# Kernel tuning notes

Measured on AMD Instinct MI355X. Metric: run time of the kernel, lower is better.

The kernel has to match this reference:

```python
import jax, jax.numpy as jnp
import numpy as np

B, S_IMG, S_TXT, S_BOK = 1, 2048, 512, 4
DM, H, DH, R = 3072, 24, 128, 16
LORA_SCALE, LORA_ALPHA, BOKEH_SCALE = 1.0, 16.0, 1.0
EPS = 1e-6


def _rms_norm(x, w):
    # normalize over head_dim (last axis), Flux RMSNorm eps=1e-6
    var = jnp.mean(jnp.square(x), axis=-1, keepdims=True)
    return x * jax.lax.rsqrt(var + EPS) * w


def _lora(x, w_down, w_up):
    # LoRALinear: up(down(x)) * alpha/rank
    return (x @ w_down.T) @ w_up.T * (LORA_ALPHA / R)


def _apply_rope(x, cos, sin):
    # x: [B,H,S,D]; cos/sin: [S,D]; diffusers use_real=True, unbind_dim=-1 (interleaved pairs)
    x1 = x[..., 0::2]
    x2 = x[..., 1::2]
    rot = jnp.stack([-x2, x1], axis=-1).reshape(x.shape)
    return x * cos[None, None] + rot * sin[None, None]


def _sdpa(q, k, v):
    # q:[B,H,Sq,D] k,v:[B,H,Sk,D]
    scale = 1.0 / jnp.sqrt(jnp.asarray(q.shape[-1], q.dtype))
    scores = jnp.einsum('bhqd,bhkd->bhqk', q, k) * scale
    p = jax.nn.softmax(scores, axis=-1)
    return jnp.einsum('bhqk,bhkd->bhqd', p, v)


def setup_inputs() -> dict:
    key = jax.random.key(0)
    ks = jax.random.split(key, 40)
    std = 0.02
    d = {}
    d['hidden_states'] = jax.random.normal(ks[0], (B, S_IMG, DM), jnp.float32)
    d['encoder_hidden_states'] = jax.random.normal(ks[1], (B, S_TXT, DM), jnp.float32)
    d['bokeh_embeds'] = jax.random.normal(ks[2], (B, S_BOK, DM), jnp.float32)
    theta = jax.random.uniform(ks[3], (S_TXT + S_IMG, DH // 2), jnp.float32) * 2 * np.pi
    theta = jnp.repeat(theta, 2, axis=-1)  # interleaved pairs share angle
    d['rope_cos'] = jnp.cos(theta)
    d['rope_sin'] = jnp.sin(theta)
    # base attention params
    for i, nm in enumerate(['Wq', 'Wk', 'Wv', 'Waq', 'Wak', 'Wav', 'Wo', 'Wao']):
        d[nm] = jax.random.normal(ks[4 + i], (DM, DM), jnp.float32) * std
    for i, nm in enumerate(['bq', 'bk', 'bv', 'baq', 'bak', 'bav', 'bo', 'bao']):
        d[nm] = jax.random.normal(ks[12 + i], (DM,), jnp.float32) * std
    for i, nm in enumerate(['norm_q_w', 'norm_k_w', 'norm_aq_w', 'norm_ak_w']):
        d[nm] = 1.0 + jax.random.normal(ks[20 + i], (DH,), jnp.float32) * std
    # LoRA adapters (up weights random, not zero, for nontrivial math)
    for i, nm in enumerate(['kb_down', 'vb_down', 'qadp_down', 'kadp_down']):
        d[nm] = jax.random.normal(ks[24 + i], (R, DM), jnp.float32) * (1.0 / R)
    for i, nm in enumerate(['kb_up', 'vb_up', 'qadp_up', 'kadp_up']):
        d[nm] = jax.random.normal(ks[28 + i], (DM, R), jnp.float32) * std
    return d


def reference(hidden_states, encoder_hidden_states, bokeh_embeds, rope_cos, rope_sin,
              Wq, Wk, Wv, Waq, Wak, Wav, Wo, Wao,
              bq, bk, bv, baq, bak, bav, bo, bao,
              norm_q_w, norm_k_w, norm_aq_w, norm_ak_w,
              kb_down, vb_down, qadp_down, kadp_down,
              kb_up, vb_up, qadp_up, kadp_up):
    Bsz = encoder_hidden_states.shape[0]

    def heads(x):  # [B,S,DM] -> [B,H,S,DH]
        return x.reshape(Bsz, -1, H, DH).transpose(0, 2, 1, 3)

    q = hidden_states @ Wq.T + bq
    k = hidden_states @ Wk.T + bk
    v = hidden_states @ Wv.T + bv
    q = q + LORA_SCALE * _lora(q, qadp_down, qadp_up)
    k = k + LORA_SCALE * _lora(k, kadp_down, kadp_up)
    q, k, v = heads(q), heads(k), heads(v)
    q = _rms_norm(q, norm_q_w)
    k = _rms_norm(k, norm_k_w)

    eq = heads(encoder_hidden_states @ Waq.T + baq)
    ek = heads(encoder_hidden_states @ Wak.T + bak)
    ev = heads(encoder_hidden_states @ Wav.T + bav)
    eq = _rms_norm(eq, norm_aq_w)
    ek = _rms_norm(ek, norm_ak_w)

    q = jnp.concatenate([eq, q], axis=2)
    k = jnp.concatenate([ek, k], axis=2)
    v = jnp.concatenate([ev, v], axis=2)

    q = _apply_rope(q, rope_cos, rope_sin)
    k = _apply_rope(k, rope_cos, rope_sin)

    out = _sdpa(q, k, v)  # [B,H,S,DH]
    out = out.transpose(0, 2, 1, 3).reshape(Bsz, -1, H * DH)

    # bokeh pass
    kd = heads(_lora(bokeh_embeds, kb_down, kb_up))
    vd = heads(_lora(bokeh_embeds, vb_down, vb_up))
    cam = _sdpa(q, kd, vd).transpose(0, 2, 1, 3).reshape(Bsz, -1, H * DH)
    out = out + BOKEH_SCALE * cam

    enc_out = out[:, :S_TXT]
    img_out = out[:, S_TXT:]
    img_out = img_out @ Wo.T + bo
    enc_out = enc_out @ Wao.T + bao
    return (img_out, enc_out)
```

## Files before the change

### kernel.cpp

```cpp
#include <hip/hip_runtime.h>

#define DMDL 3072
#define SEQ  2560
#define STXT 512
#define HEADS 24
#define DHD  128
#define WB9 9437184

typedef float f32x4 __attribute__((ext_vector_type(4)));
typedef __bf16 bf16x8 __attribute__((ext_vector_type(8)));
typedef unsigned short u16x4 __attribute__((ext_vector_type(4)));

static __device__ __forceinline__ unsigned short f2bf(float f) {
  unsigned u = __float_as_uint(f);
  u += 0x7fffu + ((u >> 16) & 1u);
  return (unsigned short)(u >> 16);
}

static __device__ __forceinline__ float fexp2(float x) {
  return __builtin_amdgcn_exp2f(x);
}

static __device__ __forceinline__ void gload16(const unsigned short* g, unsigned short* l) {
  __builtin_amdgcn_global_load_lds(
      (const __attribute__((address_space(1))) unsigned int*)g,
      (__attribute__((address_space(3))) unsigned int*)l, 16, 0, 0);
}

__global__ __launch_bounds__(256) void convf2b_kernel(
    const float* __restrict__ src, unsigned short* __restrict__ dst) {
  const int idx4 = blockIdx.x * 256 + threadIdx.x;
  float4 v = *(const float4*)(src + (size_t)idx4 * 4);
  u16x4 b = { f2bf(v.x), f2bf(v.y), f2bf(v.z), f2bf(v.w) };
  *(u16x4*)(dst + (size_t)idx4 * 4) = b;
}

__global__ __launch_bounds__(256) void convw_kernel(
    const float* __restrict__ s0, const float* __restrict__ s1,
    const float* __restrict__ s2, unsigned short* __restrict__ dst) {
  const float* src = (blockIdx.y == 0) ? s0 : (blockIdx.y == 1) ? s1 : s2;
  const size_t idx4 = (size_t)blockIdx.x * 256 + threadIdx.x;
  float4 v = *(const float4*)(src + idx4 * 4);
  u16x4 b = { f2bf(v.x), f2bf(v.y), f2bf(v.z), f2bf(v.w) };
  *(u16x4*)(dst + (size_t)blockIdx.y * WB9 + idx4 * 4) = b;
}

__device__ __forceinline__ void gemm_body(
    const unsigned short* __restrict__ A, const unsigned short* __restrict__ Bw,
    const float* __restrict__ bias, float* __restrict__ C,
    int row0, int col0) {
  __shared__ unsigned short Al[128][64];
  __shared__ unsigned short Bl[128][64];
  const int t = threadIdx.x, w = t >> 6, l = t & 63;
  const int wr = (w >> 1) << 6, wc = (w & 1) << 6;
  const int l15 = l & 15, lg = l >> 4;
  f32x4 acc[4][4];
#pragma unroll
  for (int i = 0; i < 4; i++)
#pragma unroll
    for (int j = 0; j < 4; j++) acc[i][j] = (f32x4){0.f, 0.f, 0.f, 0.f};

  for (int k0 = 0; k0 < DMDL; k0 += 64) {
    __syncthreads();
#pragma unroll
    for (int g = 0; g < 4; g++) {
      const int jb = ((w << 2) + g) << 6;
      const int jl = jb + l;
      const int row = jl >> 3, sl = jl & 7;
      const int col = ((sl ^ (row & 7)) << 3);
      gload16(A  + (size_t)(row0 + row) * DMDL + k0 + col, ((unsigned short*)Al) + (size_t)jb * 8);
      gload16(Bw + (size_t)(col0 + row) * DMDL + k0 + col, ((unsigned short*)Bl) + (size_t)jb * 8);
    }
    asm volatile("s_waitcnt vmcnt(0)" ::: "memory");
    __syncthreads();
#pragma unroll
    for (int kf = 0; kf < 2; kf++) {
      bf16x8 af[4], bfr[4];
#pragma unroll
      for (int i = 0; i < 4; i++) {
        const int ra = wr + (i << 4) + l15;
        af[i]  = *(const bf16x8*)&Al[ra][(((kf << 2) + lg) ^ (ra & 7)) << 3];
        const int rb = wc + (i << 4) + l15;
        bfr[i] = *(const bf16x8*)&Bl[rb][(((kf << 2) + lg) ^ (rb & 7)) << 3];
      }
      __builtin_amdgcn_s_setprio(1);
#pragma unroll
      for (int i = 0; i < 4; i++)
#pragma unroll
        for (int j = 0; j < 4; j++)
          acc[i][j] = __builtin_amdgcn_mfma_f32_16x16x32_bf16(af[i], bfr[j], acc[i][j], 0, 0, 0);
      __builtin_amdgcn_s_setprio(0);
    }
  }
#pragma unroll
  for (int i = 0; i < 4; i++)
#pragma unroll
    for (int j = 0; j < 4; j++) {
      const int col = col0 + wc + (j << 4) + l15;
      const float bb = bias[col];
      const int rbase = row0 + wr + (i << 4) + (lg << 2);
#pragma unroll
      for (int r2 = 0; r2 < 4; r2++)
        C[(size_t)(rbase + r2) * DMDL + col] = acc[i][j][r2] + bb;
    }
}

__global__ __launch_bounds__(256) void gemm3_kernel(
    const unsigned short* __restrict__ A, const unsigned short* __restrict__ w3,
    const float* __restrict__ b0, const float* __restrict__ b1, const float* __restrict__ b2,
    float* __restrict__ c0, float* __restrict__ c1, float* __restrict__ c2, int M) {
  const int nM = M >> 7;
  const int nwg = nM * 72;
  const int cpx = nwg >> 3;
  const int sid = (blockIdx.x & 7) * cpx + (blockIdx.x >> 3);
  const int bxx = sid / nM, by = sid - bxx * nM;
  const int grp = bxx / 24, bx = bxx - grp * 24;
  const unsigned short* Bw = w3 + (size_t)grp * WB9;
  const float* bias = (grp == 0) ? b0 : (grp == 1) ? b1 : b2;
  float* C = (grp == 0) ? c0 : (grp == 1) ? c1 : c2;
  gemm_body(A, Bw, bias, C, by << 7, bx << 7);
}

__global__ __launch_bounds__(256) void gemm_out_kernel(
    const unsigned short* __restrict__ attnbf, const unsigned short* __restrict__ w3,
    const float* __restrict__ bo, const float* __restrict__ bao,
    float* __restrict__ out) {
  const int sid = (blockIdx.x & 7) * 60 + (blockIdx.x >> 3);
  if (sid < 384) {
    const int bx = sid >> 4, by = sid & 15;
    gemm_body(attnbf + (size_t)STXT * DMDL, w3, bo, out, by << 7, bx << 7);
  } else {
    const int s2 = sid - 384;
    const int bx = s2 >> 2, by = s2 & 3;
    gemm_body(attnbf, w3 + WB9, bao, out + (size_t)2048 * DMDL, by << 7, bx << 7);
  }
}

__global__ __launch_bounds__(256) void lora_down2_kernel(
    const float* __restrict__ q0, const float* __restrict__ k0,
    const float* __restrict__ qad, const float* __restrict__ kad,
    float* __restrict__ tmpq, float* __restrict__ tmpk) {
  const int t = threadIdx.x, w = t >> 6, l = t & 63;
  const int m = blockIdx.x;
  const float* X = blockIdx.y ? k0 : q0;
  const float* dwn = blockIdx.y ? kad : qad;
  float* tmp = blockIdx.y ? tmpk : tmpq;
  const float* x = X + (size_t)m * DMDL;
  float acc[16];
#pragma unroll
  for (int r = 0; r < 16; r++) acc[r] = 0.f;
  for (int k = t; k < DMDL; k += 256) {
    float xv = x[k];
#pragma unroll
    for (int r = 0; r < 16; r++) acc[r] += xv * dwn[r * DMDL + k];
  }
#pragma unroll
  for (int off = 1; off < 64; off <<= 1)
#pragma unroll
    for (int r = 0; r < 16; r++) acc[r] += __shfl_xor(acc[r], off);
  __shared__ float red[4][16];
  if (l == 0)
#pragma unroll
    for (int r = 0; r < 16; r++) red[w][r] = acc[r];
  __syncthreads();
  if (t < 16) tmp[(size_t)m * 16 + t] = red[0][t] + red[1][t] + red[2][t] + red[3][t];
}

#define QSCALE 0.12751743f
__global__ __launch_bounds__(256) void pack_kernel(
    const float* __restrict__ q0, const float* __restrict__ k0,
    const float* __restrict__ eq, const float* __restrict__ ek,
    const float* __restrict__ tmpq, const float* __restrict__ tmpk,
    const float* __restrict__ qau, const float* __restrict__ kau,
    const float* __restrict__ nq, const float* __restrict__ nk,
    const float* __restrict__ naq, const float* __restrict__ nak,
    const float* __restrict__ rc, const float* __restrict__ rsn,
    unsigned short* __restrict__ Qp, unsigned short* __restrict__ Kp) {
  const int t = threadIdx.x, w = t >> 6, l = t & 63;
  const int s = blockIdx.x * 4 + w;
  const int h = blockIdx.y;
  const int which = blockIdx.z;
  const int n = h * DHD + 2 * l;
  float2 x;
  const float* nw;
  if (s < STXT) {
    x = *(const float2*)(((which == 0) ? eq : ek) + (size_t)s * DMDL + n);
    nw = (which == 0) ? naq : nak;
  } else {
    x = *(const float2*)(((which == 0) ? q0 : k0) + (size_t)(s - STXT) * DMDL + n);
    nw = (which == 0) ? nq : nk;
    const float* tv = ((which == 0) ? tmpq : tmpk) + (size_t)(s - STXT) * 16;
    const float* uv = ((which == 0) ? qau : kau) + (size_t)n * 16;
    float l1 = 0.f, l2 = 0.f;
#pragma unroll
    for (int r = 0; r < 16; r++) { l1 += tv[r] * uv[r]; l2 += tv[r] * uv[16 + r]; }
    x.x += l1; x.y += l2;
  }
  float ss = x.x * x.x + x.y * x.y;
#pragma unroll
  for (int off = 1; off < 64; off <<= 1) ss += __shfl_xor(ss, off);
  float inv = rsqrtf(ss * (1.f / 128.f) + 1e-6f);
  float xw1 = x.x * inv * nw[2 * l];
  float xw2 = x.y * inv * nw[2 * l + 1];
  float c1 = rc[(size_t)s * DHD + 2 * l], c2 = rc[(size_t)s * DHD + 2 * l + 1];
  float s1 = rsn[(size_t)s * DHD + 2 * l], s2 = rsn[(size_t)s * DHD + 2 * l + 1];
  float y1 = xw1 * c1 - xw2 * s1;
  float y2 = xw2 * c2 + xw1 * s2;
  if (which == 0) { y1 *= QSCALE; y2 *= QSCALE; }
  unsigned short* dst = ((which == 0) ? Qp : Kp) + ((size_t)h * SEQ + s) * DHD + 2 * l;
  unsigned pk = (unsigned)f2bf(y1) | ((unsigned)f2bf(y2) << 16);
  *(unsigned*)dst = pk;
}

__global__ __launch_bounds__(256) void vpackT_kernel(
    const float* __restrict__ v0, const float* __restrict__ ev,
    unsigned short* __restrict__ Vtg) {
  __shared__ unsigned short tile[64][136];
  const int t = threadIdx.x;
  const int s0 = blockIdx.x << 6;
  const int h = blockIdx.y;
  const float* src;
  int srow;
  if (s0 < STXT) { src = ev; srow = s0; } else { src = v0; srow = s0 - STXT; }
#pragma unroll
  for (int p = 0; p < 8; p++) {
    int idx4 = (p << 8) + t;
    int r = idx4 >> 5, c4 = idx4 & 31;
    float4 v = *(const float4*)(src + (size_t)(srow + r) * DMDL + h * DHD + (c4 << 2));
    u16x4 b = { f2bf(v.x), f2bf(v.y), f2bf(v.z), f2bf(v.w) };
    *(u16x4*)&tile[r][c4 << 2] = b;
  }
  __syncthreads();
  const int d = t >> 1, sc = (t & 1) << 5;
  unsigned short outv[32];
#pragma unroll
  for (int e = 0; e < 32; e++) outv[e] = tile[sc + e][d];
  unsigned short* dst = Vtg + ((size_t)h * DHD + d) * SEQ + s0 + sc;
#pragma unroll
  for (int q = 0; q < 4; q++)
    *(uint4*)(dst + (q << 3)) = *(uint4*)&outv[q << 3];
}

__global__ __launch_bounds__(256) void bokeh_down_kernel(
    const float* __restrict__ bok, const float* __restrict__ kbd,
    const float* __restrict__ vbd, float* __restrict__ tkv) {
  const int t = threadIdx.x, w = t >> 6, l = t & 63;
  const int mat = blockIdx.x >> 2, j = blockIdx.x & 3;
  const float* dwn = mat ? vbd : kbd;
  const float* x = bok + (size_t)j * DMDL;
  float acc[16];
#pragma unroll
  for (int r = 0; r < 16; r++) acc[r] = 0.f;
  for (int k = t; k < DMDL; k += 256) {
    float xv = x[k];
#pragma unroll
    for (int r = 0; r < 16; r++) acc[r] += xv * dwn[r * DMDL + k];
  }
#pragma unroll
  for (int off = 1; off < 64; off <<= 1)
#pragma unroll
    for (int r = 0; r < 16; r++) acc[r] += __shfl_xor(acc[r], off);
  __shared__ float red[4][16];
  if (l == 0)
#pragma unroll
    for (int r = 0; r < 16; r++) red[w][r] = acc[r];
  __syncthreads();
  if (t < 16) tkv[(mat * 4 + j) * 16 + t] = red[0][t] + red[1][t] + red[2][t] + red[3][t];
}

__global__ __launch_bounds__(256) void bokeh_up_kernel(
    const float* __restrict__ tkv, const float* __restrict__ kbu,
    const float* __restrict__ vbu, float* __restrict__ kdvd) {
  const int idx = blockIdx.x * 256 + threadIdx.x;
  const int mat = idx / 12288, rem = idx % 12288;
  const int j = rem / DMDL, n = rem % DMDL;
  const float* up = mat ? vbu : kbu;
  const float* tv = tkv + (mat * 4 + j) * 16;
  float s = 0.f;
#pragma unroll
  for (int r = 0; r < 16; r++) s += tv[r] * up[(size_t)n * 16 + r];
  kdvd[(size_t)(mat * 4 + j) * DMDL + n] = s;
}

__global__ __launch_bounds__(256) void attn_kernel(
    const unsigned short* __restrict__ Qp, const unsigned short* __restrict__ Kp,
    const unsigned short* __restrict__ Vtg, const float* __restrict__ kdvd,
    unsigned short* __restrict__ attnbf) {
  __shared__ unsigned short Klds[128][128];
  __shared__ unsigned short Vt[128][128];
  __shared__ unsigned short Pl[4][2048];
  const int t = threadIdx.x, w = t >> 6, l = t & 63;
  const int l15 = l & 15, lg = l >> 4;
  const int h = blockIdx.y;
  const int q0r = blockIdx.x * 64;
  const unsigned short* Qh = Qp + (size_t)h * SEQ * DHD;
  const unsigned short* Kh = Kp + (size_t)h * SEQ * DHD;
  const unsigned short* Vh = Vtg + (size_t)h * DHD * SEQ;
  char* Pw = (char*)&Pl[w][0];

  bf16x8 qf[4];
  {
    const unsigned short* qsrc = Qh + (size_t)(q0r + w * 16 + l15) * DHD + (lg << 3);
#pragma unroll
    for (int kf = 0; kf < 4; kf++) qf[kf] = *(const bf16x8*)(qsrc + kf * 32);
  }
  f32x4 o[8];
#pragma unroll
  for (int nc = 0; nc < 8; nc++) o[nc] = (f32x4){0.f, 0.f, 0.f, 0.f};
  float m = -1e30f, sum = 0.f;

  for (int kv0 = 0; kv0 < SEQ; kv0 += 128) {
    __syncthreads();
#pragma unroll
    for (int g = 0; g < 8; g++) {
      const int jb = ((g << 2) + w) << 6;
      const int jl = jb + l;
      const int row = jl >> 4, sl = jl & 15;
      const int col = (sl ^ (row & 7)) << 3;
      gload16(Kh + (size_t)(kv0 + row) * DHD + col, ((unsigned short*)Klds) + (size_t)jb * 8);
      gload16(Vh + (size_t)row * SEQ + kv0 + col, ((unsigned short*)Vt) + (size_t)jb * 8);
    }
    asm volatile("s_waitcnt vmcnt(0)" ::: "memory");
    __syncthreads();
    f32x4 sacc[8];
    __builtin_amdgcn_s_setprio(1);
#pragma unroll
    for (int c = 0; c < 8; c++) {
      sacc[c] = (f32x4){0.f, 0.f, 0.f, 0.f};
      const int krow = c * 16 + l15;
#pragma unroll
      for (int kf = 0; kf < 4; kf++) {
        bf16x8 kb = *(const bf16x8*)&Klds[krow][(((kf << 2) + lg) ^ (krow & 7)) << 3];
        sacc[c] = __builtin_amdgcn_mfma_f32_16x16x32_bf16(kb, qf[kf], sacc[c], 0, 0, 0);
      }
    }
    __builtin_amdgcn_s_setprio(0);
    float cm[8];
#pragma unroll
    for (int c = 0; c < 8; c++)
      cm[c] = fmaxf(fmaxf(sacc[c][0], sacc[c][1]), fmaxf(sacc[c][2], sacc[c][3]));
    float pmax = fmaxf(fmaxf(fmaxf(cm[0], cm[1]), fmaxf(cm[2], cm[3])),
                       fmaxf(fmaxf(cm[4], cm[5]), fmaxf(cm[6], cm[7])));
    pmax = fmaxf(pmax, __shfl_xor(pmax, 16));
    pmax = fmaxf(pmax, __shfl_xor(pmax, 32));
    const bool skip = __all(pmax <= m + 8.f);
    const float mnew = skip ? m : fmaxf(m, pmax);
    float ps = 0.f;
#pragma unroll
    for (int c = 0; c < 8; c++) {
      float p0 = fexp2(sacc[c][0] - mnew);
      float p1 = fexp2(sacc[c][1] - mnew);
      float p2 = fexp2(sacc[c][2] - mnew);
      float p3 = fexp2(sacc[c][3] - mnew);
      ps += (p0 + p1) + (p2 + p3);
      unsigned lo, hi;
      asm("v_cvt_pk_bf16_f32 %0, %1, %2" : "=v"(lo) : "v"(p0), "v"(p1));
      asm("v_cvt_pk_bf16_f32 %0, %1, %2" : "=v"(hi) : "v"(p2), "v"(p3));
      const int byteoff = (l15 << 8) + (((((c << 1) + (lg >> 1)) ^ (l15 & 7))) << 4) + ((lg & 1) << 3);
      *(uint2*)(Pw + byteoff) = make_uint2(lo, hi);
    }
    ps += __shfl_xor(ps, 16);
    ps += __shfl_xor(ps, 32);
    if (!skip) {
      const float sc = fexp2(m - mnew);
      sum = sum * sc + ps;
      m = mnew;
      float s0 = __shfl(sc, (lg << 2) + 0);
      float s1 = __shfl(sc, (lg << 2) + 1);
      float s2 = __shfl(sc, (lg << 2) + 2);
      float s3 = __shfl(sc, (lg << 2) + 3);
#pragma unroll
      for (int nc = 0; nc < 8; nc++) {
        o[nc][0] *= s0; o[nc][1] *= s1; o[nc][2] *= s2; o[nc][3] *= s3;
      }
    } else {
      sum += ps;
    }
    __builtin_amdgcn_s_setprio(1);
#pragma unroll
    for (int kf2 = 0; kf2 < 4; kf2++) {
      bf16x8 pa = *(const bf16x8*)(Pw + (l15 << 8) + ((((kf2 << 2) + lg) ^ (l15 & 7)) << 4));
#pragma unroll
      for (int nc = 0; nc < 8; nc++) {
        const int vrow = nc * 16 + l15;
        bf16x8 vb = *(const bf16x8*)&Vt[vrow][(((kf2 << 2) + lg) ^ (vrow & 7)) << 3];
        o[nc] = __builtin_amdgcn_mfma_f32_16x16x32_bf16(pa, vb, o[nc], 0, 0, 0);
      }
    }
    __builtin_amdgcn_s_setprio(0);
  }

  float rinv[4];
  {
    float su0 = __shfl(sum, (lg << 2) + 0);
    float su1 = __shfl(sum, (lg << 2) + 1);
    float su2 = __shfl(sum, (lg << 2) + 2);
    float su3 = __shfl(sum, (lg << 2) + 3);
    rinv[0] = 1.f / su0; rinv[1] = 1.f / su1; rinv[2] = 1.f / su2; rinv[3] = 1.f / su3;
  }

  __syncthreads();
  float* kdl = (float*)&Klds[0][0];
  {
    const int j8 = t >> 5, d4 = (t & 31) << 2;
    *(float4*)&kdl[j8 * 128 + d4] = *(const float4*)(kdvd + (size_t)j8 * DMDL + h * DHD + d4);
  }
  __syncthreads();
  float q32[4][8];
#pragma unroll
  for (int kf = 0; kf < 4; kf++)
#pragma unroll
    for (int r = 0; r < 8; r++) q32[kf][r] = (float)qf[kf][r];
  float pj[4];
#pragma unroll
  for (int jb = 0; jb < 4; jb++) {
    float d = 0.f;
#pragma unroll
    for (int kf = 0; kf < 4; kf++)
#pragma unroll
      for (int r = 0; r < 8; r++)
        d += q32[kf][r] * kdl[jb * 128 + (kf << 5) + (lg << 3) + r];
    d += __shfl_xor(d, 16);
    d += __shfl_xor(d, 32);
    pj[jb] = d;
  }
  float cmx = fmaxf(fmaxf(pj[0], pj[1]), fmaxf(pj[2], pj[3]));
  float cs = 0.f;
#pragma unroll
  for (int jb = 0; jb < 4; jb++) { pj[jb] = fexp2(pj[jb] - cmx); cs += pj[jb]; }
  float ci = 1.f / cs;
#pragma unroll
  for (int jb = 0; jb < 4; jb++) pj[jb] *= ci;
  float* pnl = kdl + 1024 + (w << 6);
  if (lg == 0) {
#pragma unroll
    for (int jb = 0; jb < 4; jb++) pnl[l15 * 4 + jb] = pj[jb];
  }
  __syncthreads();
  float pr[4][4];
#pragma unroll
  for (int j = 0; j < 4; j++)
#pragma unroll
    for (int jb = 0; jb < 4; jb++) pr[j][jb] = pnl[(((lg << 2) + j) << 2) + jb];
  const float* vdl = kdl + 512;
#pragma unroll
  for (int nc = 0; nc < 8; nc++) {
    const int col = (nc << 4) + l15;
#pragma unroll
    for (int j = 0; j < 4; j++) {
      float cam = pr[j][0] * vdl[col] + pr[j][1] * vdl[128 + col] +
                  pr[j][2] * vdl[256 + col] + pr[j][3] * vdl[384 + col];
      float outv = o[nc][j] * rinv[j] + cam;
      const int row = q0r + (w << 4) + (lg << 2) + j;
      attnbf[(size_t)row * DMDL + h * DHD + col] = f2bf(outv);
    }
  }
}

extern "C" void kernel_launch(void* const* d_in, const int* in_sizes, int n_in,
                              void* d_out, int out_size, void* d_ws, size_t ws_size,
                              hipStream_t stream) {
  (void)in_sizes; (void)n_in; (void)out_size; (void)ws_size;
  const float* hs  = (const float*)d_in[0];
  const float* enc = (const float*)d_in[1];
  const float* bok = (const float*)d_in[2];
  const float* rc  = (const float*)d_in[3];
  const float* rsn = (const float*)d_in[4];
  const float* Wq  = (const float*)d_in[5];
  const float* Wk  = (const float*)d_in[6];
  const float* Wv  = (const float*)d_in[7];
  const float* Waq = (const float*)d_in[8];
  const float* Wak = (const float*)d_in[9];
  const float* Wav = (const float*)d_in[10];
  const float* Wo  = (const float*)d_in[11];
  const float* Wao = (const float*)d_in[12];
  const float* bq  = (const float*)d_in[13];
  const float* bk  = (const float*)d_in[14];
  const float* bv  = (const float*)d_in[15];
  const float* baq = (const float*)d_in[16];
  const float* bak = (const float*)d_in[17];
  const float* bav = (const float*)d_in[18];
  const float* bo  = (const float*)d_in[19];
  const float* bao = (const float*)d_in[20];
  const float* nq  = (const float*)d_in[21];
  const float* nk  = (const float*)d_in[22];
  const float* naq = (const float*)d_in[23];
  const float* nak = (const float*)d_in[24];
  const float* kbd = (const float*)d_in[25];
  const float* vbd = (const float*)d_in[26];
  const float* qad = (const float*)d_in[27];
  const float* kad = (const float*)d_in[28];
  const float* kbu = (const float*)d_in[29];
  const float* vbu = (const float*)d_in[30];
  const float* qau = (const float*)d_in[31];
  const float* kau = (const float*)d_in[32];

  char* ws = (char*)d_ws;
  unsigned short* w3     = (unsigned short*)(ws + 0);
  unsigned short* hs_bf  = (unsigned short*)(ws + 56623104);
  unsigned short* enc_bf = (unsigned short*)(ws + 69206016);
  float* q0   = (float*)(ws + 72351744);
  float* k0   = (float*)(ws + 97517568);
  float* v0   = (float*)(ws + 122683392);
  float* eq   = (float*)(ws + 147849216);
  float* ek   = (float*)(ws + 154140672);
  float* ev   = (float*)(ws + 160432128);
  float* tmpq = (float*)(ws + 166723584);
  float* tmpk = (float*)(ws + 166854656);
  float* tkv  = (float*)(ws + 166985728);
  float* kdvd = (float*)(ws + 166986240);
  unsigned short* Qp  = (unsigned short*)(ws + 167084544);
  unsigned short* Kp  = (unsigned short*)(ws + 182813184);
  unsigned short* Vtg = (unsigned short*)(ws + 72351744);
  unsigned short* attnbf = (unsigned short*)(ws + 122683392);

  float* out = (float*)d_out;

  dim3 blk(256);

  convf2b_kernel<<<6144, blk, 0, stream>>>(hs, hs_bf);
  convf2b_kernel<<<1536, blk, 0, stream>>>(enc, enc_bf);
  bokeh_down_kernel<<<8, blk, 0, stream>>>(bok, kbd, vbd, tkv);
  bokeh_up_kernel<<<96, blk, 0, stream>>>(tkv, kbu, vbu, kdvd);

  convw_kernel<<<dim3(9216, 3), blk, 0, stream>>>(Wq, Wk, Wv, w3);
  gemm3_kernel<<<1152, blk, 0, stream>>>(hs_bf, w3, bq, bk, bv, q0, k0, v0, 2048);
  convw_kernel<<<dim3(9216, 3), blk, 0, stream>>>(Waq, Wak, Wav, w3);
  gemm3_kernel<<<288, blk, 0, stream>>>(enc_bf, w3, baq, bak, bav, eq, ek, ev, 512);

  lora_down2_kernel<<<dim3(2048, 2), blk, 0, stream>>>(q0, k0, qad, kad, tmpq, tmpk);

  pack_kernel<<<dim3(SEQ / 4, HEADS, 2), blk, 0, stream>>>(
      q0, k0, eq, ek, tmpq, tmpk, qau, kau, nq, nk, naq, nak, rc, rsn, Qp, Kp);
  vpackT_kernel<<<dim3(SEQ / 64, HEADS), blk, 0, stream>>>(v0, ev, Vtg);

  attn_kernel<<<dim3(SEQ / 64, HEADS), blk, 0, stream>>>(Qp, Kp, Vtg, kdvd, attnbf);

  convw_kernel<<<dim3(9216, 2), blk, 0, stream>>>(Wo, Wao, Wao, w3);
  gemm_out_kernel<<<480, blk, 0, stream>>>(attnbf, w3, bo, bao, out);
}
```

Baseline: 680.8 us.

## Fuse V transpose into QKV GEMM epilogue and double query rows per attention block

The V projection GEMM now writes bf16 straight into the transposed head-major V layout, so the separate vpackT kernel and the fp32 v/ev buffers are no longer needed. The attention kernel now handles 128 query rows per block, two 16-row sub-blocks per wave, which halves the grid and reuses each K/V tile loaded into LDS across twice as many queries. The workspace layout is rearranged to fit these buffers. In exchange the epilogue stores are strided 8-byte writes, and the doubled accumulators raise register pressure, which may reduce attention occupancy.

```diff
diff --git a/kernel.cpp b/kernel.cpp
--- a/kernel.cpp
+++ b/kernel.cpp
@@ -45,9 +45,11 @@
   *(u16x4*)(dst + (size_t)blockIdx.y * WB9 + idx4 * 4) = b;
 }
 
-__device__ __forceinline__ void gemm_body(
+template <int VMODE>
+__device__ __forceinline__ void gemm_body_t(
     const unsigned short* __restrict__ A, const unsigned short* __restrict__ Bw,
     const float* __restrict__ bias, float* __restrict__ C,
+    unsigned short* __restrict__ VT, int s_base,
     int row0, int col0) {
   __shared__ unsigned short Al[128][64];
   __shared__ unsigned short Bl[128][64];
@@ -99,16 +101,23 @@
       const int col = col0 + wc + (j << 4) + l15;
       const float bb = bias[col];
       const int rbase = row0 + wr + (i << 4) + (lg << 2);
-#pragma unroll
-      for (int r2 = 0; r2 < 4; r2++)
-        C[(size_t)(rbase + r2) * DMDL + col] = acc[i][j][r2] + bb;
+      if constexpr (VMODE == 0) {
+#pragma unroll
+        for (int r2 = 0; r2 < 4; r2++)
+          C[(size_t)(rbase + r2) * DMDL + col] = acc[i][j][r2] + bb;
+      } else {
+        u16x4 v4 = { f2bf(acc[i][j][0] + bb), f2bf(acc[i][j][1] + bb),
+                     f2bf(acc[i][j][2] + bb), f2bf(acc[i][j][3] + bb) };
+        *(u16x4*)(VT + (size_t)col * SEQ + s_base + rbase) = v4;
+      }
     }
 }
 
 __global__ __launch_bounds__(256) void gemm3_kernel(
     const unsigned short* __restrict__ A, const unsigned short* __restrict__ w3,
     const float* __restrict__ b0, const float* __restrict__ b1, const float* __restrict__ b2,
-    float* __restrict__ c0, float* __restrict__ c1, float* __restrict__ c2, int M) {
+    float* __restrict__ c0, float* __restrict__ c1, unsigned short* __restrict__ vt,
+    int M, int s_base) {
   const int nM = M >> 7;
   const int nwg = nM * 72;
   const int cpx = nwg >> 3;
@@ -116,9 +125,12 @@
   const int bxx = sid / nM, by = sid - bxx * nM;
   const int grp = bxx / 24, bx = bxx - grp * 24;
   const unsigned short* Bw = w3 + (size_t)grp * WB9;
-  const float* bias = (grp == 0) ? b0 : (grp == 1) ? b1 : b2;
-  float* C = (grp == 0) ? c0 : (grp == 1) ? c1 : c2;
-  gemm_body(A, Bw, bias, C, by << 7, bx << 7);
+  if (grp == 0)
+    gemm_body_t<0>(A, Bw, b0, c0, nullptr, 0, by << 7, bx << 7);
+  else if (grp == 1)
+    gemm_body_t<0>(A, Bw, b1, c1, nullptr, 0, by << 7, bx << 7);
+  else
+    gemm_body_t<1>(A, Bw, b2, nullptr, vt, s_base, by << 7, bx << 7);
 }
 
 __global__ __launch_bounds__(256) void gemm_out_kernel(
@@ -128,11 +140,11 @@
   const int sid = (blockIdx.x & 7) * 60 + (blockIdx.x >> 3);
   if (sid < 384) {
     const int bx = sid >> 4, by = sid & 15;
-    gemm_body(attnbf + (size_t)STXT * DMDL, w3, bo, out, by << 7, bx << 7);
+    gemm_body_t<0>(attnbf + (size_t)STXT * DMDL, w3, bo, out, nullptr, 0, by << 7, bx << 7);
   } else {
     const int s2 = sid - 384;
     const int bx = s2 >> 2, by = s2 & 3;
-    gemm_body(attnbf, w3 + WB9, bao, out + (size_t)2048 * DMDL, by << 7, bx << 7);
+    gemm_body_t<0>(attnbf, w3 + WB9, bao, out + (size_t)2048 * DMDL, nullptr, 0, by << 7, bx << 7);
   }
 }
 
@@ -212,35 +224,6 @@
   *(unsigned*)dst = pk;
 }
 
-__global__ __launch_bounds__(256) void vpackT_kernel(
-    const float* __restrict__ v0, const float* __restrict__ ev,
-    unsigned short* __restrict__ Vtg) {
-  __shared__ unsigned short tile[64][136];
-  const int t = threadIdx.x;
-  const int s0 = blockIdx.x << 6;
-  const int h = blockIdx.y;
-  const float* src;
-  int srow;
-  if (s0 < STXT) { src = ev; srow = s0; } else { src = v0; srow = s0 - STXT; }
-#pragma unroll
-  for (int p = 0; p < 8; p++) {
-    int idx4 = (p << 8) + t;
-    int r = idx4 >> 5, c4 = idx4 & 31;
-    float4 v = *(const float4*)(src + (size_t)(srow + r) * DMDL + h * DHD + (c4 << 2));
-    u16x4 b = { f2bf(v.x), f2bf(v.y), f2bf(v.z), f2bf(v.w) };
-    *(u16x4*)&tile[r][c4 << 2] = b;
-  }
-  __syncthreads();
-  const int d = t >> 1, sc = (t & 1) << 5;
-  unsigned short outv[32];
-#pragma unroll
-  for (int e = 0; e < 32; e++) outv[e] = tile[sc + e][d];
-  unsigned short* dst = Vtg + ((size_t)h * DHD + d) * SEQ + s0 + sc;
-#pragma unroll
-  for (int q = 0; q < 4; q++)
-    *(uint4*)(dst + (q << 3)) = *(uint4*)&outv[q << 3];
-}
-
 __global__ __launch_bounds__(256) void bokeh_down_kernel(
     const float* __restrict__ bok, const float* __restrict__ kbd,
     const float* __restrict__ vbd, float* __restrict__ tkv) {
@@ -292,22 +275,26 @@
   const int t = threadIdx.x, w = t >> 6, l = t & 63;
   const int l15 = l & 15, lg = l >> 4;
   const int h = blockIdx.y;
-  const int q0r = blockIdx.x * 64;
+  const int q0r = blockIdx.x * 128;
   const unsigned short* Qh = Qp + (size_t)h * SEQ * DHD;
   const unsigned short* Kh = Kp + (size_t)h * SEQ * DHD;
   const unsigned short* Vh = Vtg + (size_t)h * DHD * SEQ;
   char* Pw = (char*)&Pl[w][0];
 
-  bf16x8 qf[4];
-  {
-    const unsigned short* qsrc = Qh + (size_t)(q0r + w * 16 + l15) * DHD + (lg << 3);
-#pragma unroll
-    for (int kf = 0; kf < 4; kf++) qf[kf] = *(const bf16x8*)(qsrc + kf * 32);
-  }
-  f32x4 o[8];
-#pragma unroll
-  for (int nc = 0; nc < 8; nc++) o[nc] = (f32x4){0.f, 0.f, 0.f, 0.f};
-  float m = -1e30f, sum = 0.f;
+  bf16x8 qf2[2][4];
+#pragma unroll
+  for (int hb = 0; hb < 2; hb++) {
+    const unsigned short* qsrc = Qh + (size_t)(q0r + w * 32 + hb * 16 + l15) * DHD + (lg << 3);
+#pragma unroll
+    for (int kf = 0; kf < 4; kf++) qf2[hb][kf] = *(const bf16x8*)(qsrc + kf * 32);
+  }
+  f32x4 o2[2][8];
+#pragma unroll
+  for (int hb = 0; hb < 2; hb++)
+#pragma unroll
+    for (int nc = 0; nc < 8; nc++) o2[hb][nc] = (f32x4){0.f, 0.f, 0.f, 0.f};
+  float m2[2] = {-1e30f, -1e30f};
+  float sum2[2] = {0.f, 0.f};
 
   for (int kv0 = 0; kv0 < SEQ; kv0 += 128) {
     __syncthreads();
@@ -322,81 +309,88 @@
     }
     asm volatile("s_waitcnt vmcnt(0)" ::: "memory");
     __syncthreads();
-    f32x4 sacc[8];
-    __builtin_amdgcn_s_setprio(1);
-#pragma unroll
-    for (int c = 0; c < 8; c++) {
-      sacc[c] = (f32x4){0.f, 0.f, 0.f, 0.f};
-      const int krow = c * 16 + l15;
-#pragma unroll
-      for (int kf = 0; kf < 4; kf++) {
-        bf16x8 kb = *(const bf16x8*)&Klds[krow][(((kf << 2) + lg) ^ (krow & 7)) << 3];
-        sacc[c] = __builtin_amdgcn_mfma_f32_16x16x32_bf16(kb, qf[kf], sacc[c], 0, 0, 0);
-      }
-    }
-    __builtin_amdgcn_s_setprio(0);
-    float cm[8];
-#pragma unroll
-    for (int c = 0; c < 8; c++)
-      cm[c] = fmaxf(fmaxf(sacc[c][0], sacc[c][1]), fmaxf(sacc[c][2], sacc[c][3]));
-    float pmax = fmaxf(fmaxf(fmaxf(cm[0], cm[1]), fmaxf(cm[2], cm[3])),
-                       fmaxf(fmaxf(cm[4], cm[5]), fmaxf(cm[6], cm[7])));
-    pmax = fmaxf(pmax, __shfl_xor(pmax, 16));
-    pmax = fmaxf(pmax, __shfl_xor(pmax, 32));
-    const bool skip = __all(pmax <= m + 8.f);
-    const float mnew = skip ? m : fmaxf(m, pmax);
-    float ps = 0.f;
-#pragma unroll
-    for (int c = 0; c < 8; c++) {
-      float p0 = fexp2(sacc[c][0] - mnew);
-      float p1 = fexp2(sacc[c][1] - mnew);
-      float p2 = fexp2(sacc[c][2] - mnew);
-      float p3 = fexp2(sacc[c][3] - mnew);
-      ps += (p0 + p1) + (p2 + p3);
-      unsigned lo, hi;
-      asm("v_cvt_pk_bf16_f32 %0, %1, %2" : "=v"(lo) : "v"(p0), "v"(p1));
-      asm("v_cvt_pk_bf16_f32 %0, %1, %2" : "=v"(hi) : "v"(p2), "v"(p3));
-      const int byteoff = (l15 << 8) + (((((c << 1) + (lg >> 1)) ^ (l15 & 7))) << 4) + ((lg & 1) << 3);
-      *(uint2*)(Pw + byteoff) = make_uint2(lo, hi);
-    }
-    ps += __shfl_xor(ps, 16);
-    ps += __shfl_xor(ps, 32);
-    if (!skip) {
-      const float sc = fexp2(m - mnew);
-      sum = sum * sc + ps;
-      m = mnew;
-      float s0 = __shfl(sc, (lg << 2) + 0);
-      float s1 = __shfl(sc, (lg << 2) + 1);
-      float s2 = __shfl(sc, (lg << 2) + 2);
-      float s3 = __shfl(sc, (lg << 2) + 3);
-#pragma unroll
-      for (int nc = 0; nc < 8; nc++) {
-        o[nc][0] *= s0; o[nc][1] *= s1; o[nc][2] *= s2; o[nc][3] *= s3;
-      }
-    } else {
-      sum += ps;
-    }
-    __builtin_amdgcn_s_setprio(1);
-#pragma unroll
-    for (int kf2 = 0; kf2 < 4; kf2++) {
-      bf16x8 pa = *(const bf16x8*)(Pw + (l15 << 8) + ((((kf2 << 2) + lg) ^ (l15 & 7)) << 4));
-#pragma unroll
-      for (int nc = 0; nc < 8; nc++) {
-        const int vrow = nc * 16 + l15;
-        bf16x8 vb = *(const bf16x8*)&Vt[vrow][(((kf2 << 2) + lg) ^ (vrow & 7)) << 3];
-        o[nc] = __builtin_amdgcn_mfma_f32_16x16x32_bf16(pa, vb, o[nc], 0, 0, 0);
-      }
-    }
-    __builtin_amdgcn_s_setprio(0);
-  }
-
-  float rinv[4];
-  {
-    float su0 = __shfl(sum, (lg << 2) + 0);
-    float su1 = __shfl(sum, (lg << 2) + 1);
-    float su2 = __shfl(sum, (lg << 2) + 2);
-    float su3 = __shfl(sum, (lg << 2) + 3);
-    rinv[0] = 1.f / su0; rinv[1] = 1.f / su1; rinv[2] = 1.f / su2; rinv[3] = 1.f / su3;
+
+#pragma unroll
+    for (int hb = 0; hb < 2; hb++) {
+      f32x4 sacc[8];
+      __builtin_amdgcn_s_setprio(1);
+#pragma unroll
+      for (int c = 0; c < 8; c++) {
+        sacc[c] = (f32x4){0.f, 0.f, 0.f, 0.f};
+        const int krow = c * 16 + l15;
+#pragma unroll
+        for (int kf = 0; kf < 4; kf++) {
+          bf16x8 kb = *(const bf16x8*)&Klds[krow][(((kf << 2) + lg) ^ (krow & 7)) << 3];
+          sacc[c] = __builtin_amdgcn_mfma_f32_16x16x32_bf16(kb, qf2[hb][kf], sacc[c], 0, 0, 0);
+        }
+      }
+      __builtin_amdgcn_s_setprio(0);
+      float cm[8];
+#pragma unroll
+      for (int c = 0; c < 8; c++)
+        cm[c] = fmaxf(fmaxf(sacc[c][0], sacc[c][1]), fmaxf(sacc[c][2], sacc[c][3]));
+      float pmax = fmaxf(fmaxf(fmaxf(cm[0], cm[1]), fmaxf(cm[2], cm[3])),
+                         fmaxf(fmaxf(cm[4], cm[5]), fmaxf(cm[6], cm[7])));
+      pmax = fmaxf(pmax, __shfl_xor(pmax, 16));
+      pmax = fmaxf(pmax, __shfl_xor(pmax, 32));
+      const bool skip = __all(pmax <= m2[hb] + 8.f);
+      const float mnew = skip ? m2[hb] : fmaxf(m2[hb], pmax);
+      float ps = 0.f;
+#pragma unroll
+      for (int c = 0; c < 8; c++) {
+        float p0 = fexp2(sacc[c][0] - mnew);
+        float p1 = fexp2(sacc[c][1] - mnew);
+        float p2 = fexp2(sacc[c][2] - mnew);
+        float p3 = fexp2(sacc[c][3] - mnew);
+        ps += (p0 + p1) + (p2 + p3);
+        unsigned lo, hi;
+        asm("v_cvt_pk_bf16_f32 %0, %1, %2" : "=v"(lo) : "v"(p0), "v"(p1));
+        asm("v_cvt_pk_bf16_f32 %0, %1, %2" : "=v"(hi) : "v"(p2), "v"(p3));
+        const int byteoff = (l15 << 8) + (((((c << 1) + (lg >> 1)) ^ (l15 & 7))) << 4) + ((lg & 1) << 3);
+        *(uint2*)(Pw + byteoff) = make_uint2(lo, hi);
+      }
+      ps += __shfl_xor(ps, 16);
+      ps += __shfl_xor(ps, 32);
+      if (!skip) {
+        const float sc = fexp2(m2[hb] - mnew);
+        sum2[hb] = sum2[hb] * sc + ps;
+        m2[hb] = mnew;
+        float s0 = __shfl(sc, (lg << 2) + 0);
+        float s1 = __shfl(sc, (lg << 2) + 1);
+        float s2 = __shfl(sc, (lg << 2) + 2);
+        float s3 = __shfl(sc, (lg << 2) + 3);
+#pragma unroll
+        for (int nc = 0; nc < 8; nc++) {
+          o2[hb][nc][0] *= s0; o2[hb][nc][1] *= s1;
+          o2[hb][nc][2] *= s2; o2[hb][nc][3] *= s3;
+        }
+      } else {
+        sum2[hb] += ps;
+      }
+      __builtin_amdgcn_s_setprio(1);
+#pragma unroll
+      for (int kf2 = 0; kf2 < 4; kf2++) {
+        bf16x8 pa = *(const bf16x8*)(Pw + (l15 << 8) + ((((kf2 << 2) + lg) ^ (l15 & 7)) << 4));
+#pragma unroll
+        for (int nc = 0; nc < 8; nc++) {
+          const int vrow = nc * 16 + l15;
+          bf16x8 vb = *(const bf16x8*)&Vt[vrow][(((kf2 << 2) + lg) ^ (vrow & 7)) << 3];
+          o2[hb][nc] = __builtin_amdgcn_mfma_f32_16x16x32_bf16(pa, vb, o2[hb][nc], 0, 0, 0);
+        }
+      }
+      __builtin_amdgcn_s_setprio(0);
+    }
+  }
+
+  float rinv2[2][4];
+#pragma unroll
+  for (int hb = 0; hb < 2; hb++) {
+    float su0 = __shfl(sum2[hb], (lg << 2) + 0);
+    float su1 = __shfl(sum2[hb], (lg << 2) + 1);
+    float su2 = __shfl(sum2[hb], (lg << 2) + 2);
+    float su3 = __shfl(sum2[hb], (lg << 2) + 3);
+    rinv2[hb][0] = 1.f / su0; rinv2[hb][1] = 1.f / su1;
+    rinv2[hb][2] = 1.f / su2; rinv2[hb][3] = 1.f / su3;
   }
 
   __syncthreads();
@@ -406,53 +400,60 @@
     *(float4*)&kdl[j8 * 128 + d4] = *(const float4*)(kdvd + (size_t)j8 * DMDL + h * DHD + d4);
   }
   __syncthreads();
-  float q32[4][8];
-#pragma unroll
-  for (int kf = 0; kf < 4; kf++)
-#pragma unroll
-    for (int r = 0; r < 8; r++) q32[kf][r] = (float)qf[kf][r];
-  float pj[4];
-#pragma unroll
-  for (int jb = 0; jb < 4; jb++) {
-    float d = 0.f;
+#pragma unroll
+  for (int hb = 0; hb < 2; hb++) {
+    float q32[4][8];
 #pragma unroll
     for (int kf = 0; kf < 4; kf++)
 #pragma unroll
-      for (int r = 0; r < 8; r++)
-        d += q32[kf][r] * kdl[jb * 128 + (kf << 5) + (lg << 3) + r];
-    d += __shfl_xor(d, 16);
-    d += __shfl_xor(d, 32);
-    pj[jb] = d;
-  }
-  float cmx = fmaxf(fmaxf(pj[0], pj[1]), fmaxf(pj[2], pj[3]));
-  float cs = 0.f;
-#pragma unroll
-  for (int jb = 0; jb < 4; jb++) { pj[jb] = fexp2(pj[jb] - cmx); cs += pj[jb]; }
-  float ci = 1.f / cs;
-#pragma unroll
-  for (int jb = 0; jb < 4; jb++) pj[jb] *= ci;
-  float* pnl = kdl + 1024 + (w << 6);
-  if (lg == 0) {
-#pragma unroll
-    for (int jb = 0; jb < 4; jb++) pnl[l15 * 4 + jb] = pj[jb];
+      for (int r = 0; r < 8; r++) q32[kf][r] = (float)qf2[hb][kf][r];
+    float pj[4];
+#pragma unroll
+    for (int jb = 0; jb < 4; jb++) {
+      float d = 0.f;
+#pragma unroll
+      for (int kf = 0; kf < 4; kf++)
+#pragma unroll
+        for (int r = 0; r < 8; r++)
+          d += q32[kf][r] * kdl[jb * 128 + (kf << 5) + (lg << 3) + r];
+      d += __shfl_xor(d, 16);
+      d += __shfl_xor(d, 32);
+      pj[jb] = d;
+    }
+    float cmx = fmaxf(fmaxf(pj[0], pj[1]), fmaxf(pj[2], pj[3]));
+    float cs = 0.f;
+#pragma unroll
+    for (int jb = 0; jb < 4; jb++) { pj[jb] = fexp2(pj[jb] - cmx); cs += pj[jb]; }
+    float ci = 1.f / cs;
+#pragma unroll
+    for (int jb = 0; jb < 4; jb++) pj[jb] *= ci;
+    float* pnl = kdl + 1024 + (w << 7) + (hb << 6);
+    if (lg == 0) {
+#pragma unroll
+      for (int jb = 0; jb < 4; jb++) pnl[l15 * 4 + jb] = pj[jb];
+    }
   }
   __syncthreads();
-  float pr[4][4];
-#pragma unroll
-  for (int j = 0; j < 4; j++)
-#pragma unroll
-    for (int jb = 0; jb < 4; jb++) pr[j][jb] = pnl[(((lg << 2) + j) << 2) + jb];
   const float* vdl = kdl + 512;
 #pragma unroll
-  for (int nc = 0; nc < 8; nc++) {
-    const int col = (nc << 4) + l15;
-#pragma unroll
-    for (int j = 0; j < 4; j++) {
-      float cam = pr[j][0] * vdl[col] + pr[j][1] * vdl[128 + col] +
-                  pr[j][2] * vdl[256 + col] + pr[j][3] * vdl[384 + col];
-      float outv = o[nc][j] * rinv[j] + cam;
-      const int row = q0r + (w << 4) + (lg << 2) + j;
-      attnbf[(size_t)row * DMDL + h * DHD + col] = f2bf(outv);
+  for (int hb = 0; hb < 2; hb++) {
+    const float* pnl = kdl + 1024 + (w << 7) + (hb << 6);
+    float pr[4][4];
+#pragma unroll
+    for (int j = 0; j < 4; j++)
+#pragma unroll
+      for (int jb = 0; jb < 4; jb++) pr[j][jb] = pnl[(((lg << 2) + j) << 2) + jb];
+#pragma unroll
+    for (int nc = 0; nc < 8; nc++) {
+      const int col = (nc << 4) + l15;
+#pragma unroll
+      for (int j = 0; j < 4; j++) {
+        float cam = pr[j][0] * vdl[col] + pr[j][1] * vdl[128 + col] +
+                    pr[j][2] * vdl[256 + col] + pr[j][3] * vdl[384 + col];
+        float outv = o2[hb][nc][j] * rinv2[hb][j] + cam;
+        const int row = q0r + (w << 5) + (hb << 4) + (lg << 2) + j;
+        attnbf[(size_t)row * DMDL + h * DHD + col] = f2bf(outv);
+      }
     }
   }
 }
@@ -501,18 +502,16 @@
   unsigned short* enc_bf = (unsigned short*)(ws + 69206016);
   float* q0   = (float*)(ws + 72351744);
   float* k0   = (float*)(ws + 97517568);
-  float* v0   = (float*)(ws + 122683392);
-  float* eq   = (float*)(ws + 147849216);
-  float* ek   = (float*)(ws + 154140672);
-  float* ev   = (float*)(ws + 160432128);
-  float* tmpq = (float*)(ws + 166723584);
-  float* tmpk = (float*)(ws + 166854656);
-  float* tkv  = (float*)(ws + 166985728);
-  float* kdvd = (float*)(ws + 166986240);
-  unsigned short* Qp  = (unsigned short*)(ws + 167084544);
-  unsigned short* Kp  = (unsigned short*)(ws + 182813184);
-  unsigned short* Vtg = (unsigned short*)(ws + 72351744);
-  unsigned short* attnbf = (unsigned short*)(ws + 122683392);
+  unsigned short* Vtg = (unsigned short*)(ws + 122683392);
+  unsigned short* attnbf = (unsigned short*)(ws + 147849216);
+  float* eq   = (float*)(ws + 163577856);
+  float* ek   = (float*)(ws + 169869312);
+  float* tmpq = (float*)(ws + 176160768);
+  float* tmpk = (float*)(ws + 176291840);
+  float* tkv  = (float*)(ws + 176422912);
+  float* kdvd = (float*)(ws + 176423424);
+  unsigned short* Qp  = (unsigned short*)(ws + 176521728);
+  unsigned short* Kp  = (unsigned short*)(ws + 192250368);
 
   float* out = (float*)d_out;
 
@@ -524,17 +523,16 @@
   bokeh_up_kernel<<<96, blk, 0, stream>>>(tkv, kbu, vbu, kdvd);
 
   convw_kernel<<<dim3(9216, 3), blk, 0, stream>>>(Wq, Wk, Wv, w3);
-  gemm3_kernel<<<1152, blk, 0, stream>>>(hs_bf, w3, bq, bk, bv, q0, k0, v0, 2048);
+  gemm3_kernel<<<1152, blk, 0, stream>>>(hs_bf, w3, bq, bk, bv, q0, k0, Vtg, 2048, STXT);
   convw_kernel<<<dim3(9216, 3), blk, 0, stream>>>(Waq, Wak, Wav, w3);
-  gemm3_kernel<<<288, blk, 0, stream>>>(enc_bf, w3, baq, bak, bav, eq, ek, ev, 512);
+  gemm3_kernel<<<288, blk, 0, stream>>>(enc_bf, w3, baq, bak, bav, eq, ek, Vtg, 512, 0);
 
   lora_down2_kernel<<<dim3(2048, 2), blk, 0, stream>>>(q0, k0, qad, kad, tmpq, tmpk);
 
   pack_kernel<<<dim3(SEQ / 4, HEADS, 2), blk, 0, stream>>>(
       q0, k0, eq, ek, tmpq, tmpk, qau, kau, nq, nk, naq, nak, rc, rsn, Qp, Kp);
-  vpackT_kernel<<<dim3(SEQ / 64, HEADS), blk, 0, stream>>>(v0, ev, Vtg);
-
-  attn_kernel<<<dim3(SEQ / 64, HEADS), blk, 0, stream>>>(Qp, Kp, Vtg, kdvd, attnbf);
+
+  attn_kernel<<<dim3(SEQ / 128, HEADS), blk, 0, stream>>>(Qp, Kp, Vtg, kdvd, attnbf);
 
   convw_kernel<<<dim3(9216, 2), blk, 0, stream>>>(Wo, Wao, Wao, w3);
   gemm_out_kernel<<<480, blk, 0, stream>>>(attnbf, w3, bo, bao, out);
```

Result: slower. 776.9 us (+14.1%).

## Double-buffer K/V tiles in attention with 64-wide KV blocks

Applied to the files above, without the earlier changes.

The attention kernel now splits the KV loop into 64-column tiles held in two LDS buffers, prefetching the next tile with async global-to-LDS loads while computing on the current one. This is meant to hide global load latency that was previously exposed by a load-wait-sync at the start of every 128-wide iteration. LDS footprint stays about the same, but there are twice as many iterations, each running the online-softmax max/rescale bookkeeping, plus one barrier per iteration. The Klds buffer is reused for the bokeh epilogue.

```diff
diff --git a/kernel.cpp b/kernel.cpp
--- a/kernel.cpp
+++ b/kernel.cpp
@@ -286,9 +286,9 @@
     const unsigned short* __restrict__ Qp, const unsigned short* __restrict__ Kp,
     const unsigned short* __restrict__ Vtg, const float* __restrict__ kdvd,
     unsigned short* __restrict__ attnbf) {
-  __shared__ unsigned short Klds[128][128];
-  __shared__ unsigned short Vt[128][128];
-  __shared__ unsigned short Pl[4][2048];
+  __shared__ unsigned short Klds[2][64][128];
+  __shared__ unsigned short Vt[2][128][64];
+  __shared__ unsigned short Pl[4][1024];
   const int t = threadIdx.x, w = t >> 6, l = t & 63;
   const int l15 = l & 15, lg = l >> 4;
   const int h = blockIdx.y;
@@ -309,45 +309,59 @@
   for (int nc = 0; nc < 8; nc++) o[nc] = (f32x4){0.f, 0.f, 0.f, 0.f};
   float m = -1e30f, sum = 0.f;
 
-  for (int kv0 = 0; kv0 < SEQ; kv0 += 128) {
-    __syncthreads();
-#pragma unroll
-    for (int g = 0; g < 8; g++) {
-      const int jb = ((g << 2) + w) << 6;
-      const int jl = jb + l;
-      const int row = jl >> 4, sl = jl & 15;
-      const int col = (sl ^ (row & 7)) << 3;
-      gload16(Kh + (size_t)(kv0 + row) * DHD + col, ((unsigned short*)Klds) + (size_t)jb * 8);
-      gload16(Vh + (size_t)row * SEQ + kv0 + col, ((unsigned short*)Vt) + (size_t)jb * 8);
-    }
-    asm volatile("s_waitcnt vmcnt(0)" ::: "memory");
-    __syncthreads();
-    f32x4 sacc[8];
+#define ASTAGE(buf, kvb)                                                        \
+  {                                                                             \
+    _Pragma("unroll")                                                           \
+    for (int g = 0; g < 4; g++) {                                               \
+      const int jb = (g << 2) + w;                                              \
+      const int jl = (jb << 6) + l;                                             \
+      {                                                                         \
+        const int row = jl >> 4, sl = jl & 15;                                  \
+        const int col = (sl ^ (row & 7)) << 3;                                  \
+        gload16(Kh + (size_t)((kvb) + row) * DHD + col,                         \
+                &Klds[buf][0][0] + (jb << 9));                                  \
+      }                                                                         \
+      {                                                                         \
+        const int row = jl >> 3, sl = jl & 7;                                   \
+        const int col = (sl ^ (row & 7)) << 3;                                  \
+        gload16(Vh + (size_t)row * SEQ + (kvb) + col,                           \
+                &Vt[buf][0][0] + (jb << 9));                                    \
+      }                                                                         \
+    }                                                                           \
+  }
+
+  ASTAGE(0, 0)
+  asm volatile("s_waitcnt vmcnt(0)" ::: "memory");
+  __syncthreads();
+  int cur = 0;
+
+  for (int kv0 = 0; kv0 < SEQ; kv0 += 64) {
+    if (kv0 + 64 < SEQ) ASTAGE(cur ^ 1, kv0 + 64)
+    f32x4 sacc[4];
     __builtin_amdgcn_s_setprio(1);
 #pragma unroll
-    for (int c = 0; c < 8; c++) {
+    for (int c = 0; c < 4; c++) {
       sacc[c] = (f32x4){0.f, 0.f, 0.f, 0.f};
       const int krow = c * 16 + l15;
 #pragma unroll
       for (int kf = 0; kf < 4; kf++) {
-        bf16x8 kb = *(const bf16x8*)&Klds[krow][(((kf << 2) + lg) ^ (krow & 7)) << 3];
+        bf16x8 kb = *(const bf16x8*)&Klds[cur][krow][(((kf << 2) + lg) ^ (krow & 7)) << 3];
         sacc[c] = __builtin_amdgcn_mfma_f32_16x16x32_bf16(kb, qf[kf], sacc[c], 0, 0, 0);
       }
     }
     __builtin_amdgcn_s_setprio(0);
-    float cm[8];
-#pragma unroll
-    for (int c = 0; c < 8; c++)
+    float cm[4];
+#pragma unroll
+    for (int c = 0; c < 4; c++)
       cm[c] = fmaxf(fmaxf(sacc[c][0], sacc[c][1]), fmaxf(sacc[c][2], sacc[c][3]));
-    float pmax = fmaxf(fmaxf(fmaxf(cm[0], cm[1]), fmaxf(cm[2], cm[3])),
-                       fmaxf(fmaxf(cm[4], cm[5]), fmaxf(cm[6], cm[7])));
+    float pmax = fmaxf(fmaxf(cm[0], cm[1]), fmaxf(cm[2], cm[3]));
     pmax = fmaxf(pmax, __shfl_xor(pmax, 16));
     pmax = fmaxf(pmax, __shfl_xor(pmax, 32));
     const bool skip = __all(pmax <= m + 8.f);
     const float mnew = skip ? m : fmaxf(m, pmax);
     float ps = 0.f;
 #pragma unroll
-    for (int c = 0; c < 8; c++) {
+    for (int c = 0; c < 4; c++) {
       float p0 = fexp2(sacc[c][0] - mnew);
       float p1 = fexp2(sacc[c][1] - mnew);
       float p2 = fexp2(sacc[c][2] - mnew);
@@ -356,7 +370,7 @@
       unsigned lo, hi;
       asm("v_cvt_pk_bf16_f32 %0, %1, %2" : "=v"(lo) : "v"(p0), "v"(p1));
       asm("v_cvt_pk_bf16_f32 %0, %1, %2" : "=v"(hi) : "v"(p2), "v"(p3));
-      const int byteoff = (l15 << 8) + (((((c << 1) + (lg >> 1)) ^ (l15 & 7))) << 4) + ((lg & 1) << 3);
+      const int byteoff = (l15 << 7) + (((((c << 1) + (lg >> 1)) ^ (l15 & 7))) << 4) + ((lg & 1) << 3);
       *(uint2*)(Pw + byteoff) = make_uint2(lo, hi);
     }
     ps += __shfl_xor(ps, 16);
@@ -378,17 +392,21 @@
     }
     __builtin_amdgcn_s_setprio(1);
 #pragma unroll
-    for (int kf2 = 0; kf2 < 4; kf2++) {
-      bf16x8 pa = *(const bf16x8*)(Pw + (l15 << 8) + ((((kf2 << 2) + lg) ^ (l15 & 7)) << 4));
+    for (int kf2 = 0; kf2 < 2; kf2++) {
+      bf16x8 pa = *(const bf16x8*)(Pw + (l15 << 7) + ((((kf2 << 2) + lg) ^ (l15 & 7)) << 4));
 #pragma unroll
       for (int nc = 0; nc < 8; nc++) {
         const int vrow = nc * 16 + l15;
-        bf16x8 vb = *(const bf16x8*)&Vt[vrow][(((kf2 << 2) + lg) ^ (vrow & 7)) << 3];
+        bf16x8 vb = *(const bf16x8*)&Vt[cur][vrow][(((kf2 << 2) + lg) ^ (vrow & 7)) << 3];
         o[nc] = __builtin_amdgcn_mfma_f32_16x16x32_bf16(pa, vb, o[nc], 0, 0, 0);
       }
     }
     __builtin_amdgcn_s_setprio(0);
-  }
+    asm volatile("s_waitcnt vmcnt(0)" ::: "memory");
+    __syncthreads();
+    cur ^= 1;
+  }
+#undef ASTAGE
 
   float rinv[4];
   {
@@ -400,7 +418,7 @@
   }
 
   __syncthreads();
-  float* kdl = (float*)&Klds[0][0];
+  float* kdl = (float*)&Klds[0][0][0];
   {
     const int j8 = t >> 5, d4 = (t & 31) << 2;
     *(float4*)&kdl[j8 * 128 + d4] = *(const float4*)(kdvd + (size_t)j8 * DMDL + h * DHD + d4);
```

New measurement: 696.9 us. 2.4% more time.

## Double-buffer LDS tiles in GEMM body to overlap global loads with MFMA

Applied to the files above, without the earlier changes.

Splits the A and B shared-memory tiles into two buffers and prefetches the K-tile two steps ahead using direct global-to-LDS loads. Partial vmcnt waits let one stage's loads stay in flight while the current tile is consumed. The goal is to hide global load latency behind the MFMA work instead of stalling on every tile. LDS use doubles to 64KB per block, which may lower occupancy.

```diff
diff --git a/kernel.cpp b/kernel.cpp
--- a/kernel.cpp
+++ b/kernel.cpp
@@ -49,8 +49,8 @@
     const unsigned short* __restrict__ A, const unsigned short* __restrict__ Bw,
     const float* __restrict__ bias, float* __restrict__ C,
     int row0, int col0) {
-  __shared__ unsigned short Al[128][64];
-  __shared__ unsigned short Bl[128][64];
+  __shared__ unsigned short Al[2][128][64];
+  __shared__ unsigned short Bl[2][128][64];
   const int t = threadIdx.x, w = t >> 6, l = t & 63;
   const int wr = (w >> 1) << 6, wc = (w & 1) << 6;
   const int l15 = l & 15, lg = l >> 4;
@@ -60,28 +60,39 @@
 #pragma unroll
     for (int j = 0; j < 4; j++) acc[i][j] = (f32x4){0.f, 0.f, 0.f, 0.f};
 
-  for (int k0 = 0; k0 < DMDL; k0 += 64) {
-    __syncthreads();
-#pragma unroll
-    for (int g = 0; g < 4; g++) {
-      const int jb = ((w << 2) + g) << 6;
-      const int jl = jb + l;
-      const int row = jl >> 3, sl = jl & 7;
-      const int col = ((sl ^ (row & 7)) << 3);
-      gload16(A  + (size_t)(row0 + row) * DMDL + k0 + col, ((unsigned short*)Al) + (size_t)jb * 8);
-      gload16(Bw + (size_t)(col0 + row) * DMDL + k0 + col, ((unsigned short*)Bl) + (size_t)jb * 8);
-    }
-    asm volatile("s_waitcnt vmcnt(0)" ::: "memory");
-    __syncthreads();
+#define GSTAGE(buf, kt)                                                       \
+  {                                                                           \
+    const int kk = (kt) << 6;                                                 \
+    _Pragma("unroll")                                                         \
+    for (int g = 0; g < 4; g++) {                                             \
+      const int jb = ((w << 2) + g) << 6;                                     \
+      const int jl = jb + l;                                                  \
+      const int row = jl >> 3, sl = jl & 7;                                   \
+      const int col = ((sl ^ (row & 7)) << 3);                                \
+      gload16(A  + (size_t)(row0 + row) * DMDL + kk + col,                    \
+              &Al[buf][0][0] + (size_t)jb * 8);                               \
+      gload16(Bw + (size_t)(col0 + row) * DMDL + kk + col,                    \
+              &Bl[buf][0][0] + (size_t)jb * 8);                               \
+    }                                                                         \
+  }
+
+  GSTAGE(0, 0)
+  GSTAGE(1, 1)
+  asm volatile("s_waitcnt vmcnt(8)" ::: "memory");
+  __syncthreads();
+
+  const int NT = DMDL >> 6;
+  for (int kt = 0; kt < NT; kt++) {
+    const int b = kt & 1;
 #pragma unroll
     for (int kf = 0; kf < 2; kf++) {
       bf16x8 af[4], bfr[4];
 #pragma unroll
       for (int i = 0; i < 4; i++) {
         const int ra = wr + (i << 4) + l15;
-        af[i]  = *(const bf16x8*)&Al[ra][(((kf << 2) + lg) ^ (ra & 7)) << 3];
+        af[i]  = *(const bf16x8*)&Al[b][ra][(((kf << 2) + lg) ^ (ra & 7)) << 3];
         const int rb = wc + (i << 4) + l15;
-        bfr[i] = *(const bf16x8*)&Bl[rb][(((kf << 2) + lg) ^ (rb & 7)) << 3];
+        bfr[i] = *(const bf16x8*)&Bl[b][rb][(((kf << 2) + lg) ^ (rb & 7)) << 3];
       }
       __builtin_amdgcn_s_setprio(1);
 #pragma unroll
@@ -91,7 +102,17 @@
           acc[i][j] = __builtin_amdgcn_mfma_f32_16x16x32_bf16(af[i], bfr[j], acc[i][j], 0, 0, 0);
       __builtin_amdgcn_s_setprio(0);
     }
-  }
+    __syncthreads();
+    if (kt + 2 < NT) {
+      GSTAGE(b, kt + 2)
+      asm volatile("s_waitcnt vmcnt(8)" ::: "memory");
+    } else {
+      asm volatile("s_waitcnt vmcnt(0)" ::: "memory");
+    }
+    __syncthreads();
+  }
+#undef GSTAGE
+
 #pragma unroll
   for (int i = 0; i < 4; i++)
 #pragma unroll
```

New measurement: 728.2 us. +7.0%, slower.
